# Kernel optimization log

Hardware: AMD Instinct MI355X
Metric: run time of the kernel (lower is better)

Reference implementation:

```python
import jax, jax.numpy as jnp
import numpy as np

N = 50000        # nodes
E = 800000       # edges (before self loops)
IN = 128         # in_channels
HID = 32         # hidden_channels (per head)
HEADS = 4
OUT = 10         # out_channels (classes)
G = 64           # graphs in batch
NEG_SLOPE = 0.2  # PyG GATConv default leaky relu slope


def setup_inputs() -> dict:
    key = jax.random.key(0)
    ks = jax.random.split(key, 12)
    s = 0.05
    return {
        "x": jax.random.normal(ks[0], (N, IN), jnp.float32),
        "W1": jax.random.normal(ks[1], (IN, HEADS * HID), jnp.float32) * s,
        "a1_src": jax.random.normal(ks[2], (HEADS, HID), jnp.float32) * s,
        "a1_dst": jax.random.normal(ks[3], (HEADS, HID), jnp.float32) * s,
        "b1": jnp.zeros((HEADS * HID,), jnp.float32),
        "W2": jax.random.normal(ks[4], (HEADS * HID, HEADS * HID), jnp.float32) * s,
        "a2_src": jax.random.normal(ks[5], (HEADS, HID), jnp.float32) * s,
        "a2_dst": jax.random.normal(ks[6], (HEADS, HID), jnp.float32) * s,
        "b2": jnp.zeros((HEADS * HID,), jnp.float32),
        "Wl": jax.random.normal(ks[7], (HEADS * HID, OUT), jnp.float32) * s,
        "bl": jnp.zeros((OUT,), jnp.float32),
        "edge_index": jax.random.randint(ks[8], (2, E), 0, N, jnp.int32),
        "batch": jnp.sort(jax.random.randint(ks[9], (N,), 0, G, jnp.int32)),
    }


def gat_conv(x, src, dst, W, a_src, a_dst, b):
    """PyG GATConv (concat=True, self loops already in src/dst). Eval mode: no dropout."""
    n = x.shape[0]
    h = (x @ W).reshape(n, HEADS, HID)                       # [N,H,C]
    al_s = jnp.einsum('nhc,hc->nh', h, a_src)                # [N,H]
    al_d = jnp.einsum('nhc,hc->nh', h, a_dst)
    e = jax.nn.leaky_relu(al_s[src] + al_d[dst], NEG_SLOPE)  # [Etot,H]
    # segment softmax over destination node neighborhoods
    m = jax.ops.segment_max(e, dst, num_segments=n)
    m = jnp.where(jnp.isfinite(m), m, 0.0)
    p = jnp.exp(e - m[dst])
    z = jax.ops.segment_sum(p, dst, num_segments=n)
    alpha = p / (z[dst] + 1e-16)                             # [Etot,H]
    out = jax.ops.segment_sum(h[src] * alpha[:, :, None], dst, num_segments=n)
    return out.reshape(n, HEADS * HID) + b


def reference(x, W1, a1_src, a1_dst, b1, W2, a2_src, a2_dst, b2, Wl, bl,
              edge_index, batch):
    n = x.shape[0]
    loops = jnp.arange(n, dtype=edge_index.dtype)
    src = jnp.concatenate([edge_index[0], loops])
    dst = jnp.concatenate([edge_index[1], loops])

    h = jax.nn.elu(gat_conv(x, src, dst, W1, a1_src, a1_dst, b1))
    h = gat_conv(h, src, dst, W2, a2_src, a2_dst, b2)

    # global_mean_pool over graph ids
    counts = jax.ops.segment_sum(jnp.ones((n,), h.dtype), batch, num_segments=G)
    pooled = jax.ops.segment_sum(h, batch, num_segments=G) / jnp.maximum(counts, 1.0)[:, None]

    logits = pooled @ Wl + bl
    return jax.nn.softmax(logits, axis=1)
```

## Files before the change

### kernel.cpp

```cpp
#include <hip/hip_runtime.h>
#include <hip/hip_bf16.h>
#include <math.h>

#define HEADS 4
#define HID 32
#define FDIM 128
#define OUTC 10
#define NEG 0.2f

typedef __attribute__((ext_vector_type(4))) float f32x4;
typedef __attribute__((ext_vector_type(8))) short bf16x8;

static __device__ __forceinline__ float lrelu(float v) { return v > 0.f ? v : NEG * v; }

static __device__ __forceinline__ unsigned bfr(float f) {
  unsigned u = __float_as_uint(f);
  return (u + 0x7fffu + ((u >> 16) & 1u)) >> 16;
}
static __device__ __forceinline__ float blo(unsigned u) { return __uint_as_float(u << 16); }
static __device__ __forceinline__ float bhi(unsigned u) { return __uint_as_float(u & 0xffff0000u); }


#define CHUNK 4096

__global__ __launch_bounds__(256) void k_bhist(
    const int* __restrict__ ei, int* __restrict__ gbc, int E, int n, int nb) {
  __shared__ int h[256];
  h[threadIdx.x] = 0;
  __syncthreads();
  int base = blockIdx.x * CHUNK;
  int tot = E + n;
  #pragma unroll
  for (int r = 0; r < 16; ++r) {
    int e = base + r * 256 + threadIdx.x;
    if (e < tot) {
      int dst = (e < E) ? ei[E + e] : (e - E);
      atomicAdd(&h[dst >> 8], 1);
    }
  }
  __syncthreads();
  if (threadIdx.x < nb && h[threadIdx.x]) atomicAdd(&gbc[threadIdx.x], h[threadIdx.x]);
}

__global__ void k_bscan(const int* __restrict__ gbc, int* __restrict__ bbase,
                        int* __restrict__ gbcur, int nb) {
  __shared__ int sh[256];
  int v = (threadIdx.x < nb) ? gbc[threadIdx.x] : 0;
  sh[threadIdx.x] = v;
  __syncthreads();
  #pragma unroll
  for (int off = 1; off < 256; off <<= 1) {
    int t = (threadIdx.x >= off) ? sh[threadIdx.x - off] : 0;
    __syncthreads();
    sh[threadIdx.x] += t;
    __syncthreads();
  }
  int excl = sh[threadIdx.x] - v;
  if (threadIdx.x <= nb) bbase[threadIdx.x] = excl;
  if (threadIdx.x < nb) gbcur[threadIdx.x] = excl;
}

__global__ __launch_bounds__(256) void k_bin(
    const int* __restrict__ ei, int* __restrict__ gbcur,
    int2* __restrict__ bbuf, int E, int n) {
  __shared__ int h[256];
  __shared__ int cur[256];
  h[threadIdx.x] = 0;
  __syncthreads();
  int base = blockIdx.x * CHUNK;
  int tot = E + n;
  #pragma unroll
  for (int r = 0; r < 16; ++r) {
    int e = base + r * 256 + threadIdx.x;
    if (e < tot) {
      int dst = (e < E) ? ei[E + e] : (e - E);
      atomicAdd(&h[dst >> 8], 1);
    }
  }
  __syncthreads();
  if (h[threadIdx.x]) cur[threadIdx.x] = atomicAdd(&gbcur[threadIdx.x], h[threadIdx.x]);
  __syncthreads();
  #pragma unroll
  for (int r = 0; r < 16; ++r) {
    int e = base + r * 256 + threadIdx.x;
    if (e < tot) {
      int src = (e < E) ? ei[e] : (e - E);
      int dst = (e < E) ? ei[E + e] : (e - E);
      int pos = atomicAdd(&cur[dst >> 8], 1);
      bbuf[pos] = make_int2(src, dst);
    }
  }
}

__global__ __launch_bounds__(256) void k_build(
    const int2* __restrict__ bbuf, const int* __restrict__ bbase,
    int* __restrict__ offs, int* __restrict__ csr, int n, int nb) {
  __shared__ int deg[256];
  __shared__ int sc[256];
  __shared__ int cur[256];
  int b = blockIdx.x;
  int ebeg = bbase[b], eend = bbase[b + 1];
  deg[threadIdx.x] = 0;
  __syncthreads();
  for (int i = ebeg + threadIdx.x; i < eend; i += 256)
    atomicAdd(&deg[bbuf[i].y & 255], 1);
  __syncthreads();
  int v = deg[threadIdx.x];
  sc[threadIdx.x] = v;
  __syncthreads();
  #pragma unroll
  for (int off = 1; off < 256; off <<= 1) {
    int t = (threadIdx.x >= off) ? sc[threadIdx.x - off] : 0;
    __syncthreads();
    sc[threadIdx.x] += t;
    __syncthreads();
  }
  int excl = sc[threadIdx.x] - v;
  int dst0 = b * 256 + threadIdx.x;
  if (dst0 < n) offs[dst0] = ebeg + excl;
  if (b == 0 && threadIdx.x == 0) offs[n] = bbase[nb];
  cur[threadIdx.x] = ebeg + excl;
  __syncthreads();
  for (int i = ebeg + threadIdx.x; i < eend; i += 256) {
    int2 sd = bbuf[i];
    int pos = atomicAdd(&cur[sd.y & 255], 1);
    csr[pos] = sd.x;
  }
}

__global__ void k_wa(const float* __restrict__ W1, const float* __restrict__ W2,
                     const float* __restrict__ a1s, const float* __restrict__ a1d,
                     const float* __restrict__ a2s, const float* __restrict__ a2d,
                     float* __restrict__ Wa) {
  int layer = blockIdx.y;
  const float* W = layer ? W2 : W1;
  int c = blockIdx.x;
  int k = threadIdx.x;
  int h = c & 3;
  const float* av = (c < 4 ? (layer ? a2s : a1s) : (layer ? a2d : a1d)) + h * 32;
  const float* wr = W + (size_t)k * 128 + h * 32;
  float s = 0.f;
  #pragma unroll
  for (int j = 0; j < 32; j += 4) {
    float4 wv = *reinterpret_cast<const float4*>(wr + j);
    float4 a4 = *reinterpret_cast<const float4*>(av + j);
    s += wv.x * a4.x + wv.y * a4.y + wv.z * a4.z + wv.w * a4.w;
  }
  Wa[layer * 1024 + k * 8 + c] = s;
}

__global__ void k_prep(const float* __restrict__ W1, const float* __restrict__ W2,
                       const float* __restrict__ Wa, uint4* __restrict__ WF) {
  int layer = blockIdx.y;
  const float* W = layer ? W2 : W1;
  const float* wa = Wa + layer * 1024;
  int gid = blockIdx.x * 256 + threadIdx.x;
  if (gid >= 2304) return;
  int lane = gid & 63, frag = gid >> 6;
  int t = frag / 9, ct = frag - t * 9;
  int quad = lane >> 4, r = lane & 15;
  int kbase = t * 32 + quad * 8;
  unsigned v[8];
  if (ct < 8) {
    int col = ct * 16 + r;
    #pragma unroll
    for (int j = 0; j < 8; ++j) v[j] = bfr(W[(size_t)(kbase + j) * 128 + col]);
  } else if (r < 8) {
    #pragma unroll
    for (int j = 0; j < 8; ++j) v[j] = bfr(wa[(kbase + j) * 8 + r]);
  } else {
    #pragma unroll
    for (int j = 0; j < 8; ++j) v[j] = 0;
  }
  uint4 pk;
  pk.x = v[0] | (v[1] << 16);
  pk.y = v[2] | (v[3] << 16);
  pk.z = v[4] | (v[5] << 16);
  pk.w = v[6] | (v[7] << 16);
  WF[layer * 2304 + gid] = pk;
}

__global__ __launch_bounds__(256) void k_mm(
    const float* __restrict__ X, const uint4* __restrict__ WF,
    unsigned short* __restrict__ H, float* __restrict__ AL, int n) {
  __shared__ uint4 wf[2304];
  int tid = threadIdx.x;
  #pragma unroll
  for (int i = 0; i < 9; ++i) wf[i * 256 + tid] = WF[i * 256 + tid];
  __syncthreads();
  int lane = tid & 63, wid = tid >> 6;
  int quad = lane >> 4, r = lane & 15;
  int rowbase = blockIdx.x * 64 + wid * 16;
  int arow = rowbase + r;
  int arowc = arow < n ? arow : 0;
  const float* xp = X + (size_t)arowc * 128 + quad * 8;
  const bf16x8* wfs = (const bf16x8*)wf;

  f32x4 acc[9];
  #pragma unroll
  for (int ct = 0; ct < 9; ++ct) acc[ct] = 0;

  #pragma unroll
  for (int t = 0; t < 4; ++t) {
    float4 x0 = *reinterpret_cast<const float4*>(xp + t * 32);
    float4 x1 = *reinterpret_cast<const float4*>(xp + t * 32 + 4);
    bf16x8 a;
    a[0] = (short)bfr(x0.x); a[1] = (short)bfr(x0.y);
    a[2] = (short)bfr(x0.z); a[3] = (short)bfr(x0.w);
    a[4] = (short)bfr(x1.x); a[5] = (short)bfr(x1.y);
    a[6] = (short)bfr(x1.z); a[7] = (short)bfr(x1.w);
    #pragma unroll
    for (int ct = 0; ct < 9; ++ct)
      acc[ct] = __builtin_amdgcn_mfma_f32_16x16x32_bf16(
          a, wfs[(t * 9 + ct) * 64 + lane], acc[ct], 0, 0, 0);
  }

  int orow0 = rowbase + quad * 4;
  #pragma unroll
  for (int rr = 0; rr < 4; ++rr) {
    int orow = orow0 + rr;
    if (orow < n) {
      unsigned short* hp = H + (size_t)orow * 128 + r;
      #pragma unroll
      for (int ct = 0; ct < 8; ++ct) hp[ct * 16] = (unsigned short)bfr(acc[ct][rr]);
      if (r < 8) AL[(size_t)orow * 8 + r] = acc[8][rr];
    }
  }
}

template<bool ELU_OUT, bool POOL>
__global__ __launch_bounds__(256) void k_agg(
    const unsigned short* __restrict__ H, const float* __restrict__ AL,
    const int* __restrict__ offs, const int* __restrict__ csr,
    const float* __restrict__ bias, float* __restrict__ OUT,
    const int* __restrict__ batch, float* __restrict__ pooled,
    int* __restrict__ gcnt, int n) {
  __shared__ int s_l[16][16];
  __shared__ float p_l[16][16][4];
  __shared__ float o_l[POOL ? 16 : 1][POOL ? 132 : 1];
  __shared__ int g_l[16];
  int tid = threadIdx.x;
  int lane = tid & 63;
  int wid = tid >> 6;
  int r = lane & 15;
  int gg = wid * 4 + (lane >> 4);
  int node = blockIdx.x * 16 + gg;
  bool nvalid = node < n;
  int nodec = nvalid ? node : 0;
  int beg = offs[nodec];
  int end = nvalid ? offs[nodec + 1] : beg;
  float4 adv = *reinterpret_cast<const float4*>(AL + (size_t)nodec * 8 + 4);
  int hsel = r >> 2;
  const uint4* hb = reinterpret_cast<const uint4*>(H) + r;

  if (POOL && r == 0) g_l[gg] = nvalid ? batch[node] : -1;

  float z0 = 0.f, z1 = 0.f, z2 = 0.f, z3 = 0.f;
  float acc[8];
  #pragma unroll
  for (int k = 0; k < 8; ++k) acc[k] = 0.f;

  for (int cb = beg; cb < end; cb += 16) {
    int idx = cb + r;
    bool v = idx < end;
    int s = 0;
    float p0 = 0.f, p1 = 0.f, p2 = 0.f, p3 = 0.f;
    if (v) {
      s = csr[idx];
      float4 a = *reinterpret_cast<const float4*>(AL + (size_t)s * 8);
      p0 = __expf(lrelu(a.x + adv.x));
      p1 = __expf(lrelu(a.y + adv.y));
      p2 = __expf(lrelu(a.z + adv.z));
      p3 = __expf(lrelu(a.w + adv.w));
    }
    z0 += p0; z1 += p1; z2 += p2; z3 += p3;

    s_l[gg][r] = s;
    *reinterpret_cast<float4*>(&p_l[gg][r][0]) = make_float4(p0, p1, p2, p3);

    int cnt = min(16, end - cb);
    for (int j0 = 0; j0 < cnt; j0 += 4) {
      int j1 = j0 + 1, j2 = j0 + 2, j3 = j0 + 3;
      bool v1 = j1 < cnt, v2 = j2 < cnt, v3 = j3 < cnt;
      int jB = v1 ? j1 : j0, jC = v2 ? j2 : j0, jD = v3 ? j3 : j0;
      int sA = s_l[gg][j0], sB = s_l[gg][jB], sC = s_l[gg][jC], sD = s_l[gg][jD];
      float pA = p_l[gg][j0][hsel];
      float pB = v1 ? p_l[gg][jB][hsel] : 0.f;
      float pC = v2 ? p_l[gg][jC][hsel] : 0.f;
      float pD = v3 ? p_l[gg][jD][hsel] : 0.f;
      uint4 uA = hb[(size_t)sA * 16];
      uint4 uB = hb[(size_t)sB * 16];
      uint4 uC = hb[(size_t)sC * 16];
      uint4 uD = hb[(size_t)sD * 16];
      acc[0] = fmaf(pA, blo(uA.x), acc[0]); acc[1] = fmaf(pA, bhi(uA.x), acc[1]);
      acc[2] = fmaf(pA, blo(uA.y), acc[2]); acc[3] = fmaf(pA, bhi(uA.y), acc[3]);
      acc[4] = fmaf(pA, blo(uA.z), acc[4]); acc[5] = fmaf(pA, bhi(uA.z), acc[5]);
      acc[6] = fmaf(pA, blo(uA.w), acc[6]); acc[7] = fmaf(pA, bhi(uA.w), acc[7]);
      acc[0] = fmaf(pB, blo(uB.x), acc[0]); acc[1] = fmaf(pB, bhi(uB.x), acc[1]);
      acc[2] = fmaf(pB, blo(uB.y), acc[2]); acc[3] = fmaf(pB, bhi(uB.y), acc[3]);
      acc[4] = fmaf(pB, blo(uB.z), acc[4]); acc[5] = fmaf(pB, bhi(uB.z), acc[5]);
      acc[6] = fmaf(pB, blo(uB.w), acc[6]); acc[7] = fmaf(pB, bhi(uB.w), acc[7]);
      acc[0] = fmaf(pC, blo(uC.x), acc[0]); acc[1] = fmaf(pC, bhi(uC.x), acc[1]);
      acc[2] = fmaf(pC, blo(uC.y), acc[2]); acc[3] = fmaf(pC, bhi(uC.y), acc[3]);
      acc[4] = fmaf(pC, blo(uC.z), acc[4]); acc[5] = fmaf(pC, bhi(uC.z), acc[5]);
      acc[6] = fmaf(pC, blo(uC.w), acc[6]); acc[7] = fmaf(pC, bhi(uC.w), acc[7]);
      acc[0] = fmaf(pD, blo(uD.x), acc[0]); acc[1] = fmaf(pD, bhi(uD.x), acc[1]);
      acc[2] = fmaf(pD, blo(uD.y), acc[2]); acc[3] = fmaf(pD, bhi(uD.y), acc[3]);
      acc[4] = fmaf(pD, blo(uD.z), acc[4]); acc[5] = fmaf(pD, bhi(uD.z), acc[5]);
      acc[6] = fmaf(pD, blo(uD.w), acc[6]); acc[7] = fmaf(pD, bhi(uD.w), acc[7]);
    }
  }

  #pragma unroll
  for (int off = 1; off < 16; off <<= 1) {
    z0 += __shfl_xor(z0, off);
    z1 += __shfl_xor(z1, off);
    z2 += __shfl_xor(z2, off);
    z3 += __shfl_xor(z3, off);
  }
  float zh = (hsel == 0) ? z0 : (hsel == 1) ? z1 : (hsel == 2) ? z2 : z3;
  float inv = 1.f / (zh + 1e-16f);
  int f0 = r * 8;
  float4 b0 = *reinterpret_cast<const float4*>(bias + f0);
  float4 b1 = *reinterpret_cast<const float4*>(bias + f0 + 4);
  float o[8];
  o[0] = acc[0] * inv + b0.x; o[1] = acc[1] * inv + b0.y;
  o[2] = acc[2] * inv + b0.z; o[3] = acc[3] * inv + b0.w;
  o[4] = acc[4] * inv + b1.x; o[5] = acc[5] * inv + b1.y;
  o[6] = acc[6] * inv + b1.z; o[7] = acc[7] * inv + b1.w;
  if (ELU_OUT) {
    #pragma unroll
    for (int k = 0; k < 8; ++k) o[k] = o[k] > 0.f ? o[k] : expm1f(o[k]);
  }

  if (!POOL) {
    if (nvalid) {
      float* op = OUT + (size_t)node * 128 + f0;
      *reinterpret_cast<float4*>(op) = make_float4(o[0], o[1], o[2], o[3]);
      *reinterpret_cast<float4*>(op + 4) = make_float4(o[4], o[5], o[6], o[7]);
    }
  } else {
    *reinterpret_cast<float4*>(&o_l[gg][f0]) = make_float4(o[0], o[1], o[2], o[3]);
    *reinterpret_cast<float4*>(&o_l[gg][f0 + 4]) = make_float4(o[4], o[5], o[6], o[7]);
    __syncthreads();
    if (tid < 128) {
      int f = tid;
      float accp = 0.f; int cur = -1;
      #pragma unroll
      for (int i = 0; i < 16; ++i) {
        int g = g_l[i];
        if (g != cur) {
          if (cur >= 0) atomicAdd(&pooled[(size_t)cur * 128 + f], accp);
          cur = g; accp = 0.f;
        }
        if (g >= 0) accp += o_l[i][f];
      }
      if (cur >= 0) atomicAdd(&pooled[(size_t)cur * 128 + f], accp);
    } else if (tid == 128) {
      int cur = -1, c = 0;
      #pragma unroll
      for (int i = 0; i < 16; ++i) {
        int g = g_l[i];
        if (g != cur) { if (cur >= 0) atomicAdd(&gcnt[cur], c); cur = g; c = 0; }
        if (g >= 0) ++c;
      }
      if (cur >= 0) atomicAdd(&gcnt[cur], c);
    }
  }
}

__global__ void k_head(const float* __restrict__ pooled, const int* __restrict__ gcnt,
                       const float* __restrict__ Wl, const float* __restrict__ bl,
                       float* __restrict__ out) {
  int g = blockIdx.x;
  int lane = threadIdx.x;
  float cnt = fmaxf((float)gcnt[g], 1.f);
  float pA = pooled[(size_t)g * 128 + lane] / cnt;
  float pB = pooled[(size_t)g * 128 + lane + 64] / cnt;
  float l[OUTC];
  #pragma unroll
  for (int o = 0; o < OUTC; ++o) {
    float s = pA * Wl[lane * OUTC + o] + pB * Wl[(lane + 64) * OUTC + o];
    #pragma unroll
    for (int off = 32; off; off >>= 1) s += __shfl_xor(s, off);
    l[o] = s + bl[o];
  }
  float mx = l[0];
  #pragma unroll
  for (int o = 1; o < OUTC; ++o) mx = fmaxf(mx, l[o]);
  float se = 0.f;
  #pragma unroll
  for (int o = 0; o < OUTC; ++o) { l[o] = __expf(l[o] - mx); se += l[o]; }
  if (lane == 0) {
    float inv = 1.f / se;
    #pragma unroll
    for (int o = 0; o < OUTC; ++o) out[g * OUTC + o] = l[o] * inv;
  }
}

extern "C" void kernel_launch(void* const* d_in, const int* in_sizes, int n_in,
                              void* d_out, int out_size, void* d_ws, size_t ws_size,
                              hipStream_t stream) {
  const float* x   = (const float*)d_in[0];
  const float* W1  = (const float*)d_in[1];
  const float* a1s = (const float*)d_in[2];
  const float* a1d = (const float*)d_in[3];
  const float* b1  = (const float*)d_in[4];
  const float* W2  = (const float*)d_in[5];
  const float* a2s = (const float*)d_in[6];
  const float* a2d = (const float*)d_in[7];
  const float* b2  = (const float*)d_in[8];
  const float* Wl  = (const float*)d_in[9];
  const float* bl  = (const float*)d_in[10];
  const int* ei    = (const int*)d_in[11];
  const int* batch = (const int*)d_in[12];
  const int N = in_sizes[12];
  const int E = in_sizes[11] / 2;
  const int G = out_size / OUTC;
  float* out = (float*)d_out;
  (void)n_in; (void)ws_size;

  const int tot = E + N;
  const int NB = (N + 255) / 256;

  char* w = (char*)d_ws;
  auto alloc = [&](size_t bytes) { char* p = w; w += (bytes + 255) & ~(size_t)255; return (void*)p; };
  unsigned short* H = (unsigned short*)alloc((size_t)N * FDIM * sizeof(unsigned short));
  float* ACT    = (float*)alloc((size_t)N * FDIM * sizeof(float));
  float* AL     = (float*)alloc((size_t)N * 8 * sizeof(float));
  uint4* WF     = (uint4*)alloc(2 * 2304 * sizeof(uint4));
  float* Wa     = (float*)alloc(2 * 1024 * sizeof(float));
  int*   offs   = (int*)alloc((size_t)(N + 1) * sizeof(int));
  int*   csr    = (int*)alloc((size_t)tot * sizeof(int));
  int2*  bbuf   = (int2*)alloc((size_t)tot * sizeof(int2));
  int*   bbase  = (int*)alloc((size_t)(NB + 1) * sizeof(int));
  int*   gbcur  = (int*)alloc(256 * sizeof(int));
  char* z0 = w;
  int*   gbc    = (int*)alloc(256 * sizeof(int));
  int*   gcnt   = (int*)alloc((size_t)G * sizeof(int));
  float* pooled = (float*)alloc((size_t)G * FDIM * sizeof(float));
  size_t zbytes = (size_t)(w - z0);
  hipMemsetAsync(z0, 0, zbytes, stream);

  int ab4 = (tot + CHUNK - 1) / CHUNK;
  k_bhist<<<ab4, 256, 0, stream>>>(ei, gbc, E, N, NB);
  k_bscan<<<1, 256, 0, stream>>>(gbc, bbase, gbcur, NB);
  k_bin<<<ab4, 256, 0, stream>>>(ei, gbcur, bbuf, E, N);
  k_build<<<NB, 256, 0, stream>>>(bbuf, bbase, offs, csr, N, NB);

  k_wa<<<dim3(8, 2), 128, 0, stream>>>(W1, W2, a1s, a1d, a2s, a2d, Wa);
  k_prep<<<dim3(9, 2), 256, 0, stream>>>(W1, W2, Wa, WF);

  int gb = (N + 63) / 64;
  int ab = (N + 15) / 16;
  k_mm<<<gb, 256, 0, stream>>>(x, WF, H, AL, N);
  k_agg<true, false><<<ab, 256, 0, stream>>>(H, AL, offs, csr, b1, ACT, batch, pooled, gcnt, N);
  k_mm<<<gb, 256, 0, stream>>>(ACT, WF + 2304, H, AL, N);
  k_agg<false, true><<<ab, 256, 0, stream>>>(H, AL, offs, csr, b2, ACT, batch, pooled, gcnt, N);

  k_head<<<G, 64, 0, stream>>>(pooled, gcnt, Wl, bl, out);
}
```

Baseline: 243.7 us.

## Precompute per-edge attention exponentials in a separate pass and store layer-1 activations as bf16

Adds a per-edge kernel that computes exp(leaky_relu(al_src+al_dst)) into a float4 buffer indexed by CSR position. The build kernel now also records each edge's destination so that kernel can run. Aggregation reads these precomputed weights instead of gathering AL and evaluating exp inside its latency-bound loop. The intermediate activation is written as bf16 and the second matmul reads bf16 directly, halving that round trip. The price is two extra kernel launches and a 16-byte-per-edge buffer written and then read back, which may cost more traffic than it saves.

After: 255.4 us. 4.8% more time.

```diff
diff --git a/kernel.cpp b/kernel.cpp
--- a/kernel.cpp
+++ b/kernel.cpp
@@ -94,7 +94,8 @@
 
 __global__ __launch_bounds__(256) void k_build(
     const int2* __restrict__ bbuf, const int* __restrict__ bbase,
-    int* __restrict__ offs, int* __restrict__ csr, int n, int nb) {
+    int* __restrict__ offs, int* __restrict__ csr, int* __restrict__ dpos,
+    int n, int nb) {
   __shared__ int deg[256];
   __shared__ int sc[256];
   __shared__ int cur[256];
@@ -125,7 +126,25 @@
     int2 sd = bbuf[i];
     int pos = atomicAdd(&cur[sd.y & 255], 1);
     csr[pos] = sd.x;
-  }
+    dpos[pos] = sd.y;
+  }
+}
+
+__global__ __launch_bounds__(256) void k_pexp(
+    const int* __restrict__ csr, const int* __restrict__ dpos,
+    const float* __restrict__ AL, float4* __restrict__ P, int tot) {
+  int i = blockIdx.x * 256 + threadIdx.x;
+  if (i >= tot) return;
+  int s = csr[i];
+  int d = dpos[i];
+  float4 as_ = *reinterpret_cast<const float4*>(AL + (size_t)s * 8);
+  float4 ad = *reinterpret_cast<const float4*>(AL + (size_t)d * 8 + 4);
+  float4 p;
+  p.x = __expf(lrelu(as_.x + ad.x));
+  p.y = __expf(lrelu(as_.y + ad.y));
+  p.z = __expf(lrelu(as_.z + ad.z));
+  p.w = __expf(lrelu(as_.w + ad.w));
+  P[i] = p;
 }
 
 __global__ void k_wa(const float* __restrict__ W1, const float* __restrict__ W2,
@@ -180,8 +199,9 @@
   WF[layer * 2304 + gid] = pk;
 }
 
+template<bool BF16IN>
 __global__ __launch_bounds__(256) void k_mm(
-    const float* __restrict__ X, const uint4* __restrict__ WF,
+    const void* __restrict__ Xv, const uint4* __restrict__ WF,
     unsigned short* __restrict__ H, float* __restrict__ AL, int n) {
   __shared__ uint4 wf[2304];
   int tid = threadIdx.x;
@@ -193,7 +213,6 @@
   int rowbase = blockIdx.x * 64 + wid * 16;
   int arow = rowbase + r;
   int arowc = arow < n ? arow : 0;
-  const float* xp = X + (size_t)arowc * 128 + quad * 8;
   const bf16x8* wfs = (const bf16x8*)wf;
 
   f32x4 acc[9];
@@ -202,13 +221,20 @@
 
   #pragma unroll
   for (int t = 0; t < 4; ++t) {
-    float4 x0 = *reinterpret_cast<const float4*>(xp + t * 32);
-    float4 x1 = *reinterpret_cast<const float4*>(xp + t * 32 + 4);
     bf16x8 a;
-    a[0] = (short)bfr(x0.x); a[1] = (short)bfr(x0.y);
-    a[2] = (short)bfr(x0.z); a[3] = (short)bfr(x0.w);
-    a[4] = (short)bfr(x1.x); a[5] = (short)bfr(x1.y);
-    a[6] = (short)bfr(x1.z); a[7] = (short)bfr(x1.w);
+    if (BF16IN) {
+      const uint4* xp = reinterpret_cast<const uint4*>(Xv) + (size_t)arowc * 16;
+      uint4 u = xp[t * 4 + quad];
+      a = *reinterpret_cast<const bf16x8*>(&u);
+    } else {
+      const float* xp = reinterpret_cast<const float*>(Xv) + (size_t)arowc * 128 + quad * 8;
+      float4 x0 = *reinterpret_cast<const float4*>(xp + t * 32);
+      float4 x1 = *reinterpret_cast<const float4*>(xp + t * 32 + 4);
+      a[0] = (short)bfr(x0.x); a[1] = (short)bfr(x0.y);
+      a[2] = (short)bfr(x0.z); a[3] = (short)bfr(x0.w);
+      a[4] = (short)bfr(x1.x); a[5] = (short)bfr(x1.y);
+      a[6] = (short)bfr(x1.z); a[7] = (short)bfr(x1.w);
+    }
     #pragma unroll
     for (int ct = 0; ct < 9; ++ct)
       acc[ct] = __builtin_amdgcn_mfma_f32_16x16x32_bf16(
@@ -230,9 +256,9 @@
 
 template<bool ELU_OUT, bool POOL>
 __global__ __launch_bounds__(256) void k_agg(
-    const unsigned short* __restrict__ H, const float* __restrict__ AL,
+    const unsigned short* __restrict__ H, const float4* __restrict__ P,
     const int* __restrict__ offs, const int* __restrict__ csr,
-    const float* __restrict__ bias, float* __restrict__ OUT,
+    const float* __restrict__ bias, unsigned short* __restrict__ OUT,
     const int* __restrict__ batch, float* __restrict__ pooled,
     int* __restrict__ gcnt, int n) {
   __shared__ int s_l[16][16];
@@ -249,7 +275,6 @@
   int nodec = nvalid ? node : 0;
   int beg = offs[nodec];
   int end = nvalid ? offs[nodec + 1] : beg;
-  float4 adv = *reinterpret_cast<const float4*>(AL + (size_t)nodec * 8 + 4);
   int hsel = r >> 2;
   const uint4* hb = reinterpret_cast<const uint4*>(H) + r;
 
@@ -264,19 +289,15 @@
     int idx = cb + r;
     bool v = idx < end;
     int s = 0;
-    float p0 = 0.f, p1 = 0.f, p2 = 0.f, p3 = 0.f;
+    float4 p = make_float4(0.f, 0.f, 0.f, 0.f);
     if (v) {
       s = csr[idx];
-      float4 a = *reinterpret_cast<const float4*>(AL + (size_t)s * 8);
-      p0 = __expf(lrelu(a.x + adv.x));
-      p1 = __expf(lrelu(a.y + adv.y));
-      p2 = __expf(lrelu(a.z + adv.z));
-      p3 = __expf(lrelu(a.w + adv.w));
-    }
-    z0 += p0; z1 += p1; z2 += p2; z3 += p3;
+      p = P[idx];
+    }
+    z0 += p.x; z1 += p.y; z2 += p.z; z3 += p.w;
 
     s_l[gg][r] = s;
-    *reinterpret_cast<float4*>(&p_l[gg][r][0]) = make_float4(p0, p1, p2, p3);
+    *reinterpret_cast<float4*>(&p_l[gg][r][0]) = p;
 
     int cnt = min(16, end - cb);
     for (int j0 = 0; j0 < cnt; j0 += 4) {
@@ -335,9 +356,12 @@
 
   if (!POOL) {
     if (nvalid) {
-      float* op = OUT + (size_t)node * 128 + f0;
-      *reinterpret_cast<float4*>(op) = make_float4(o[0], o[1], o[2], o[3]);
-      *reinterpret_cast<float4*>(op + 4) = make_float4(o[4], o[5], o[6], o[7]);
+      uint4 pk;
+      pk.x = bfr(o[0]) | (bfr(o[1]) << 16);
+      pk.y = bfr(o[2]) | (bfr(o[3]) << 16);
+      pk.z = bfr(o[4]) | (bfr(o[5]) << 16);
+      pk.w = bfr(o[6]) | (bfr(o[7]) << 16);
+      reinterpret_cast<uint4*>(OUT)[(size_t)node * 16 + r] = pk;
     }
   } else {
     *reinterpret_cast<float4*>(&o_l[gg][f0]) = make_float4(o[0], o[1], o[2], o[3]);
@@ -426,12 +450,14 @@
   char* w = (char*)d_ws;
   auto alloc = [&](size_t bytes) { char* p = w; w += (bytes + 255) & ~(size_t)255; return (void*)p; };
   unsigned short* H = (unsigned short*)alloc((size_t)N * FDIM * sizeof(unsigned short));
-  float* ACT    = (float*)alloc((size_t)N * FDIM * sizeof(float));
+  unsigned short* ACT = (unsigned short*)alloc((size_t)N * FDIM * sizeof(unsigned short));
   float* AL     = (float*)alloc((size_t)N * 8 * sizeof(float));
+  float4* P     = (float4*)alloc((size_t)tot * sizeof(float4));
   uint4* WF     = (uint4*)alloc(2 * 2304 * sizeof(uint4));
   float* Wa     = (float*)alloc(2 * 1024 * sizeof(float));
   int*   offs   = (int*)alloc((size_t)(N + 1) * sizeof(int));
   int*   csr    = (int*)alloc((size_t)tot * sizeof(int));
+  int*   dpos   = (int*)alloc((size_t)tot * sizeof(int));
   int2*  bbuf   = (int2*)alloc((size_t)tot * sizeof(int2));
   int*   bbase  = (int*)alloc((size_t)(NB + 1) * sizeof(int));
   int*   gbcur  = (int*)alloc(256 * sizeof(int));
@@ -446,17 +472,20 @@
   k_bhist<<<ab4, 256, 0, stream>>>(ei, gbc, E, N, NB);
   k_bscan<<<1, 256, 0, stream>>>(gbc, bbase, gbcur, NB);
   k_bin<<<ab4, 256, 0, stream>>>(ei, gbcur, bbuf, E, N);
-  k_build<<<NB, 256, 0, stream>>>(bbuf, bbase, offs, csr, N, NB);
+  k_build<<<NB, 256, 0, stream>>>(bbuf, bbase, offs, csr, dpos, N, NB);
 
   k_wa<<<dim3(8, 2), 128, 0, stream>>>(W1, W2, a1s, a1d, a2s, a2d, Wa);
   k_prep<<<dim3(9, 2), 256, 0, stream>>>(W1, W2, Wa, WF);
 
   int gb = (N + 63) / 64;
   int ab = (N + 15) / 16;
-  k_mm<<<gb, 256, 0, stream>>>(x, WF, H, AL, N);
-  k_agg<true, false><<<ab, 256, 0, stream>>>(H, AL, offs, csr, b1, ACT, batch, pooled, gcnt, N);
-  k_mm<<<gb, 256, 0, stream>>>(ACT, WF + 2304, H, AL, N);
-  k_agg<false, true><<<ab, 256, 0, stream>>>(H, AL, offs, csr, b2, ACT, batch, pooled, gcnt, N);
+  int pe = (tot + 255) / 256;
+  k_mm<false><<<gb, 256, 0, stream>>>(x, WF, H, AL, N);
+  k_pexp<<<pe, 256, 0, stream>>>(csr, dpos, AL, P, tot);
+  k_agg<true, false><<<ab, 256, 0, stream>>>(H, P, offs, csr, b1, ACT, batch, pooled, gcnt, N);
+  k_mm<true><<<gb, 256, 0, stream>>>(ACT, WF + 2304, H, AL, N);
+  k_pexp<<<pe, 256, 0, stream>>>(csr, dpos, AL, P, tot);
+  k_agg<false, true><<<ab, 256, 0, stream>>>(H, P, offs, csr, b2, nullptr, batch, pooled, gcnt, N);
 
   k_head<<<G, 64, 0, stream>>>(pooled, gcnt, Wl, bl, out);
 }
```
